# Kernel tuning notes

Hardware: AMD Instinct MI355X
Metric: run time of the kernel (lower is better)

Reference implementation:

```python
import jax, jax.numpy as jnp
import numpy as np

H = 1024      # hidden_size
NH = 16       # num_attention_heads
HD = H // NH  # head_size
DF = 4096     # ff intermediate
EPS = 1e-5


def layer_norm(x, g, b):
    mu = jnp.mean(x, axis=-1, keepdims=True)
    var = jnp.var(x, axis=-1, keepdims=True)
    return (x - mu) * jax.lax.rsqrt(var + EPS) * g + b


def setup_inputs() -> dict:
    key = jax.random.key(0)
    ks = jax.random.split(key, 4)
    s = 0.02
    return {
        "x": jax.random.normal(ks[0], (2, 2048, H), dtype=jnp.float32),
        "w_qkv": jax.random.normal(ks[1], (H, 3 * H), dtype=jnp.float32) * s,
        "ln1_g": jnp.ones((H,), jnp.float32),
        "ln1_b": jnp.zeros((H,), jnp.float32),
        "w1": jax.random.normal(ks[2], (H, DF), dtype=jnp.float32) * s,
        "b1": jnp.zeros((DF,), jnp.float32),
        "w2": jax.random.normal(ks[3], (DF, H), dtype=jnp.float32) * s,
        "b2": jnp.zeros((H,), jnp.float32),
        "ln2_g": jnp.ones((H,), jnp.float32),
        "ln2_b": jnp.zeros((H,), jnp.float32),
    }


def reference(x, w_qkv, ln1_g, ln1_b, w1, b1, w2, b2, ln2_g, ln2_b):
    b, s, h = x.shape
    # --- MHSelfAttention (naive) ---
    qkv = x @ w_qkv                                   # [b, s, 3h]
    qkv = qkv.reshape(b, s, 3, NH, HD)
    q, k, v = (jnp.moveaxis(qkv, 2, 0)                # [3, b, s, nh, hd]
               .transpose(0, 1, 3, 2, 4))             # [3, b, nh, s, hd]
    # NOTE: faithful quirk — scaled by sqrt(hidden_size), not head_size
    scores = jnp.einsum('bnqd,bnkd->bnqk', q, k) / jnp.sqrt(jnp.float32(h))
    probs = jax.nn.softmax(scores, axis=-1)
    ctx = jnp.einsum('bnqk,bnkd->bnqd', probs, v)     # [b, nh, s, hd]
    attn_out = ctx.transpose(0, 2, 1, 3).reshape(b, s, h)
    # post-norm residual (dropout = identity in eval)
    x = x + layer_norm(attn_out, ln1_g, ln1_b)
    # --- FFN ---
    ff = jax.nn.relu(x @ w1 + b1) @ w2 + b2
    x = x + layer_norm(ff, ln2_g, ln2_b)
    return x
```

## Files before the change

kernel.cpp:

```cpp
#include <hip/hip_runtime.h>


typedef unsigned short u16;
typedef unsigned int u32;
typedef __bf16 bf16x8 __attribute__((ext_vector_type(8)));
typedef float f32x4 __attribute__((ext_vector_type(4)));
typedef float f32x16 __attribute__((ext_vector_type(16)));
typedef u32 u32x4 __attribute__((ext_vector_type(4)));
typedef u16 u16x4 __attribute__((ext_vector_type(4)));

__device__ __forceinline__ u16 f2b(float f) {
  u32 u = __builtin_bit_cast(u32, f);
  u += 0x7fffu + ((u >> 16) & 1u);
  return (u16)(u >> 16);
}
__device__ __forceinline__ float b2f(u16 u) {
  return __builtin_bit_cast(float, (u32)u << 16);
}

__device__ __forceinline__ u32 cvtpk(float lo, float hi) {
  u32 r;
  asm("v_cvt_pk_bf16_f32 %0, %1, %2" : "=v"(r) : "v"(lo), "v"(hi));
  return r;
}

__device__ __forceinline__ void gld_lds16(const u16* g, u16* l) {
  __builtin_amdgcn_global_load_lds(
      (const __attribute__((address_space(1))) u32*)g,
      (__attribute__((address_space(3))) u32*)l, 16, 0, 0);
}

__global__ __launch_bounds__(256) void convert_bf16_kernel(
    const float* __restrict__ in, u16* __restrict__ out) {
  const int idx = blockIdx.x * 256 + threadIdx.x;
  float4 v = ((const float4*)in)[idx];
  u16x4 o = { f2b(v.x), f2b(v.y), f2b(v.z), f2b(v.w) };
  ((u16x4*)out)[idx] = o;
}

__global__ __launch_bounds__(256) void transpose_bf16_kernel(
    const float* __restrict__ in, u16* __restrict__ out, int R, int C) {
  __shared__ float tile[32][33];
  const int cb = blockIdx.x * 32, rb = blockIdx.y * 32;
  const int c = threadIdx.x & 31;
  const int r0 = threadIdx.x >> 5;
#pragma unroll
  for (int rr = 0; rr < 32; rr += 8)
    tile[r0 + rr][c] = in[(size_t)(rb + r0 + rr) * C + cb + c];
  __syncthreads();
#pragma unroll
  for (int rr = 0; rr < 32; rr += 8)
    out[(size_t)(cb + r0 + rr) * R + rb + c] = f2b(tile[c][r0 + rr]);
}

__global__ __launch_bounds__(256) void transpose_v_kernel(
    const u16* __restrict__ qkv, u16* __restrict__ vt) {
  __shared__ u16 t[64][70];
  const int bh = blockIdx.x, st = blockIdx.y;
  const int b = bh >> 4, nh = bh & 15;
  const int s0 = st * 64;
  const int r = threadIdx.x >> 3, c = (threadIdx.x & 7) << 3;
  const u16* src = qkv + (size_t)(b * 2048 + s0) * 3072 + 2048 + nh * 64;
#pragma unroll
  for (int rr = 0; rr < 64; rr += 32)
    *(u32x4*)&t[r + rr][c] = *(const u32x4*)(src + (size_t)(r + rr) * 3072 + c);
  __syncthreads();
  u16* dst = vt + ((size_t)bh * 64) * 2048 + s0;
#pragma unroll
  for (int rr = 0; rr < 64; rr += 32) {
    const int d = r + rr;
    u16 tmp[8];
#pragma unroll
    for (int j = 0; j < 8; ++j) tmp[j] = t[c + j][d];
    *(u32x4*)(dst + (size_t)d * 2048 + c) = *(u32x4*)tmp;
  }
}

#define GT(BUF, SBUF, T2, VM)                                                 \
  {                                                                           \
    const u16(*Ab)[32] = As[BUF];                                             \
    const u16(*Bb)[32] = Bs[BUF];                                             \
    bf16x8 af[4], bfr[4];                                                     \
    _Pragma("unroll") for (int nr = 0; nr < 4; ++nr)                          \
        bfr[nr] = *(const bf16x8*)&Bb[wn * 64 + nr * 16 + l16][cRd];          \
    _Pragma("unroll") for (int mr = 0; mr < 4; ++mr)                          \
        af[mr] = *(const bf16x8*)&Ab[wm * 128 + mr * 16 + l16][cRd];          \
    if ((T2) >= 0) {                                                          \
      gld_lds16(Ag + (size_t)(T2) * 32,         &As[SBUF][w * 16][0]);        \
      gld_lds16(Ag + rstep + (size_t)(T2) * 32, &As[SBUF][128 + w * 16][0]);  \
    }                                                                         \
    asm volatile("s_waitcnt lgkmcnt(0)" ::: "memory");                        \
    __builtin_amdgcn_sched_barrier(0);                                        \
    __builtin_amdgcn_s_setprio(1);                                            \
    _Pragma("unroll") for (int mr = 0; mr < 4; ++mr)                          \
        _Pragma("unroll") for (int nr = 0; nr < 4; ++nr)                      \
            acc[mr][nr] = __builtin_amdgcn_mfma_f32_16x16x32_bf16(            \
                af[mr], bfr[nr], acc[mr][nr], 0, 0, 0);                       \
    __builtin_amdgcn_s_setprio(0);                                            \
    _Pragma("unroll") for (int mr = 0; mr < 4; ++mr)                          \
        af[mr] = *(const bf16x8*)&Ab[wm * 128 + 64 + mr * 16 + l16][cRd];     \
    if ((T2) >= 0) {                                                          \
      gld_lds16(Bg + (size_t)(T2) * 32,         &Bs[SBUF][w * 16][0]);        \
      gld_lds16(Bg + rstep + (size_t)(T2) * 32, &Bs[SBUF][128 + w * 16][0]);  \
    }                                                                         \
    asm volatile("s_waitcnt lgkmcnt(0)" ::: "memory");                        \
    __builtin_amdgcn_sched_barrier(0);                                        \
    __builtin_amdgcn_s_setprio(1);                                            \
    _Pragma("unroll") for (int mr = 0; mr < 4; ++mr)                          \
        _Pragma("unroll") for (int nr = 0; nr < 4; ++nr)                      \
            acc[4 + mr][nr] = __builtin_amdgcn_mfma_f32_16x16x32_bf16(        \
                af[mr], bfr[nr], acc[4 + mr][nr], 0, 0, 0);                   \
    __builtin_amdgcn_s_setprio(0);                                            \
    if ((VM) == 4) asm volatile("s_waitcnt vmcnt(4)" ::: "memory");           \
    else if ((VM) == 0) asm volatile("s_waitcnt vmcnt(0)" ::: "memory");      \
    if ((VM) >= 0) __builtin_amdgcn_s_barrier();                              \
  }

__global__ __launch_bounds__(512) void gemm256_kernel(
    const u16* __restrict__ A, const u16* __restrict__ Bt,
    const float* __restrict__ bias, u16* __restrict__ Cb,
    int M, int N, int K, int relu,
    u16* __restrict__ Cb1, u16* __restrict__ Cb2, u16* __restrict__ Cb3) {
  const int nN = N >> 8;
  const int lin = (blockIdx.x & 7) * ((int)gridDim.x >> 3) + (blockIdx.x >> 3);
  const int m0 = (lin / nN) << 8;
  const int n0 = (lin % nN) << 8;
  const int z = blockIdx.y;
  if (z == 1) Cb = Cb1; else if (z == 2) Cb = Cb2; else if (z == 3) Cb = Cb3;

  const int tid = threadIdx.x;
  const int w = tid >> 6, lane = tid & 63;
  const int quad = lane >> 4, l16 = lane & 15;
  const int wm = w >> 2, wn = w & 3;

  __shared__ u16 As[3][256][32];
  __shared__ u16 Bs[3][256][32];

  f32x4 acc[8][4];
#pragma unroll
  for (int i = 0; i < 8; ++i)
#pragma unroll
    for (int j = 0; j < 4; ++j) acc[i][j] = {0.f, 0.f, 0.f, 0.f};

  const int srow = lane >> 2;
  const int scol = (((lane & 3) ^ (srow & 3)) << 3);
  const u16* Ag = A + (size_t)(m0 + w * 16 + srow) * K + (size_t)z * 1024 + scol;
  const u16* Bg = Bt + (size_t)(n0 + w * 16 + srow) * K + (size_t)z * 1024 + scol;
  const size_t rstep = (size_t)128 * K;

  const int cRd = ((quad ^ (l16 & 3)) << 3);

  gld_lds16(Ag,              &As[0][w * 16][0]);
  gld_lds16(Ag + rstep,      &As[0][128 + w * 16][0]);
  gld_lds16(Bg,              &Bs[0][w * 16][0]);
  gld_lds16(Bg + rstep,      &Bs[0][128 + w * 16][0]);
  gld_lds16(Ag + 32,         &As[1][w * 16][0]);
  gld_lds16(Ag + rstep + 32, &As[1][128 + w * 16][0]);
  gld_lds16(Bg + 32,         &Bs[1][w * 16][0]);
  gld_lds16(Bg + rstep + 32, &Bs[1][128 + w * 16][0]);
  asm volatile("s_waitcnt vmcnt(4)" ::: "memory");
  __builtin_amdgcn_s_barrier();

  for (int tt = 0; tt < 10; ++tt) {
    const int t = tt * 3;
    GT(0, 2, t + 2, 4)
    GT(1, 0, t + 3, 4)
    GT(2, 1, t + 4, 4)
  }
  GT(0, 0, -1, 0)
  GT(1, 0, -1, -1)

#pragma unroll
  for (int mr = 0; mr < 8; ++mr) {
    const int row = m0 + wm * 128 + mr * 16 + quad * 4;
#pragma unroll
    for (int nr = 0; nr < 4; ++nr) {
      const int col = n0 + wn * 64 + nr * 16 + l16;
      const float bv = bias ? bias[col] : 0.f;
#pragma unroll
      for (int r = 0; r < 4; ++r) {
        float v = acc[mr][nr][r] + bv;
        if (relu) v = fmaxf(v, 0.f);
        Cb[(size_t)(row + r) * N + col] = f2b(v);
      }
    }
  }
}

__global__ __launch_bounds__(256, 4) void attn_kernel(
    const u16* __restrict__ qkv, const u16* __restrict__ vt,
    float* __restrict__ Op0, float* __restrict__ Op1,
    float* __restrict__ lpart) {
  const int bh = blockIdx.x;
  const int qt = blockIdx.y;
  const int kz = blockIdx.z;
  const int b = bh >> 4, nh = bh & 15;
  const int tid = threadIdx.x;
  const int w = tid >> 6, lane = tid & 63;
  const int l32 = lane & 31, hi = lane >> 5;
  const float c2 = 0.04508422f;

  __shared__ u16 KS[64][64];
  __shared__ u16 VS[64][64];

  const size_t rs = 3072;
  const u16* qbase = qkv + (size_t)b * 2048 * rs + nh * 64;
  const u16* kbase = qbase + 1024;
  const u16* vbase = vt + (size_t)bh * 64 * 2048;
  const int q0 = qt * 128;
  const int k0beg = kz * 1024;

  bf16x8 aq[4];
  {
    const u16* qrow = qbase + (size_t)(q0 + w * 32 + l32) * rs + hi * 8;
#pragma unroll
    for (int ds = 0; ds < 4; ++ds) {
      u32x4 v = *(const u32x4*)(qrow + ds * 16);
      u16 ti[8], to[8];
      *(u32x4*)ti = v;
#pragma unroll
      for (int j = 0; j < 8; ++j) to[j] = f2b(b2f(ti[j]) * c2);
      u32x4 pk = *(u32x4*)to;
      aq[ds] = __builtin_bit_cast(bf16x8, pk);
    }
  }

  f32x16 Oacc[2];
#pragma unroll
  for (int dn = 0; dn < 2; ++dn)
#pragma unroll
    for (int i = 0; i < 16; ++i) Oacc[dn][i] = 0.f;
  float ls[4] = {0.f, 0.f, 0.f, 0.f};

  const int srow = lane >> 3;
  const int scol = ((lane & 7) ^ srow) << 3;

#pragma unroll 1
  for (int t = 0; t < 16; ++t) {
    const int k0 = k0beg + t * 64;
    __syncthreads();
    gld_lds16(kbase + (size_t)(k0 + w * 16 + srow) * rs + scol,       &KS[w * 16][0]);
    gld_lds16(kbase + (size_t)(k0 + w * 16 + 8 + srow) * rs + scol,   &KS[w * 16 + 8][0]);
    gld_lds16(vbase + (size_t)(w * 16 + srow) * 2048 + k0 + scol,     &VS[w * 16][0]);
    gld_lds16(vbase + (size_t)(w * 16 + 8 + srow) * 2048 + k0 + scol, &VS[w * 16 + 8][0]);
    __syncthreads();

    f32x16 S[2];
#pragma unroll
    for (int jt = 0; jt < 2; ++jt)
#pragma unroll
      for (int i = 0; i < 16; ++i) S[jt][i] = 0.f;
#pragma unroll
    for (int jt = 0; jt < 2; ++jt) {
      const int krow = jt * 32 + l32;
#pragma unroll
      for (int ds = 0; ds < 4; ++ds) {
        bf16x8 kv = *(const bf16x8*)&KS[krow][((2 * ds + hi) ^ (krow & 7)) << 3];
        S[jt] = __builtin_amdgcn_mfma_f32_32x32x16_bf16(kv, aq[ds], S[jt], 0, 0, 0);
      }
    }

    bf16x8 pa[4];
#pragma unroll
    for (int jt = 0; jt < 2; ++jt) {
      float p[16];
#pragma unroll
      for (int r = 0; r < 16; ++r) {
        p[r] = exp2f(S[jt][r]);
        ls[r & 3] += p[r];
      }
#pragma unroll
      for (int bq = 0; bq < 2; ++bq) {
        u32 x0 = cvtpk(p[8 * bq + 0], p[8 * bq + 1]);
        u32 y0 = cvtpk(p[8 * bq + 4], p[8 * bq + 5]);
        u32 x1 = cvtpk(p[8 * bq + 2], p[8 * bq + 3]);
        u32 y1 = cvtpk(p[8 * bq + 6], p[8 * bq + 7]);
        asm("v_permlane32_swap_b32 %0, %1" : "+v"(x0), "+v"(y0));
        asm("v_permlane32_swap_b32 %0, %1" : "+v"(x1), "+v"(y1));
        u32x4 dw = {x0, x1, y0, y1};
        pa[2 * jt + bq] = __builtin_bit_cast(bf16x8, dw);
      }
    }

#pragma unroll
    for (int dn = 0; dn < 2; ++dn) {
      const int vrow = dn * 32 + l32;
#pragma unroll
      for (int ks = 0; ks < 4; ++ks) {
        bf16x8 vv = *(const bf16x8*)&VS[vrow][((2 * ks + hi) ^ (vrow & 7)) << 3];
        Oacc[dn] = __builtin_amdgcn_mfma_f32_32x32x16_bf16(pa[ks], vv, Oacc[dn], 0, 0, 0);
      }
    }
  }

  float lsum = (ls[0] + ls[1]) + (ls[2] + ls[3]);
  const float ltot = lsum + __shfl_xor(lsum, 32);

  float* opart = kz ? Op1 : Op0;
  float* obase = opart + (size_t)b * 2048 * 1024 + (size_t)nh * 64;
  float* lbase = lpart + (size_t)kz * 4096 * 16 + (size_t)b * 2048 * 16 + nh;
#pragma unroll
  for (int r = 0; r < 16; ++r) {
    const int qrow = q0 + w * 32 + (r & 3) + 8 * (r >> 2) + 4 * hi;
#pragma unroll
    for (int dn = 0; dn < 2; ++dn)
      obase[(size_t)qrow * 1024 + dn * 32 + l32] = Oacc[dn][r];
  }
  if (lane < 32) lbase[(size_t)(q0 + w * 32 + l32) * 16] = ltot;
}

__global__ __launch_bounds__(256) void ln_attn_kernel(
    const float* __restrict__ O0, const float* __restrict__ O1,
    const float* __restrict__ l0, const float* __restrict__ l1,
    const float* __restrict__ xres, const float* __restrict__ g,
    const float* __restrict__ bb, float* __restrict__ outf,
    u16* __restrict__ outb) {
  const int row = blockIdx.x;
  const int tid = threadIdx.x;
  const int w = tid >> 6, lane = tid & 63;
  const int head = tid >> 4;
  float4 a0 = ((const float4*)(O0 + (size_t)row * 1024))[tid];
  float4 a1 = ((const float4*)(O1 + (size_t)row * 1024))[tid];
  const float inv = 1.f / (l0[row * 16 + head] + l1[row * 16 + head]);
  float4 v;
  v.x = (a0.x + a1.x) * inv;
  v.y = (a0.y + a1.y) * inv;
  v.z = (a0.z + a1.z) * inv;
  v.w = (a0.w + a1.w) * inv;
  float s = v.x + v.y + v.z + v.w;
  float s2 = v.x * v.x + v.y * v.y + v.z * v.z + v.w * v.w;
#pragma unroll
  for (int off = 32; off > 0; off >>= 1) {
    s += __shfl_xor(s, off);
    s2 += __shfl_xor(s2, off);
  }
  __shared__ float red[8];
  if (lane == 0) { red[w] = s; red[4 + w] = s2; }
  __syncthreads();
  s = red[0] + red[1] + red[2] + red[3];
  s2 = red[4] + red[5] + red[6] + red[7];
  const float mu = s * (1.f / 1024.f);
  const float var = s2 * (1.f / 1024.f) - mu * mu;
  const float rstd = rsqrtf(var + 1e-5f);
  float4 xr = ((const float4*)(xres + (size_t)row * 1024))[tid];
  float4 gv = ((const float4*)g)[tid];
  float4 bv = ((const float4*)bb)[tid];
  float4 o;
  o.x = xr.x + (v.x - mu) * rstd * gv.x + bv.x;
  o.y = xr.y + (v.y - mu) * rstd * gv.y + bv.y;
  o.z = xr.z + (v.z - mu) * rstd * gv.z + bv.z;
  o.w = xr.w + (v.w - mu) * rstd * gv.w + bv.w;
  ((float4*)(outf + (size_t)row * 1024))[tid] = o;
  u16x4 ob = { f2b(o.x), f2b(o.y), f2b(o.z), f2b(o.w) };
  *(u16x4*)(outb + (size_t)row * 1024 + (size_t)tid * 4) = ob;
}

__global__ __launch_bounds__(256) void ln_ffn_kernel(
    const u16* __restrict__ p0, const u16* __restrict__ p1,
    const u16* __restrict__ p2, const u16* __restrict__ p3,
    const float* __restrict__ bias, const float* __restrict__ xres,
    const float* __restrict__ g, const float* __restrict__ bb,
    float* __restrict__ outf) {
  const int row = blockIdx.x;
  const int tid = threadIdx.x;
  const int w = tid >> 6, lane = tid & 63;
  u16x4 a0 = ((const u16x4*)(p0 + (size_t)row * 1024))[tid];
  u16x4 a1 = ((const u16x4*)(p1 + (size_t)row * 1024))[tid];
  u16x4 a2 = ((const u16x4*)(p2 + (size_t)row * 1024))[tid];
  u16x4 a3 = ((const u16x4*)(p3 + (size_t)row * 1024))[tid];
  float4 bv4 = ((const float4*)bias)[tid];
  float4 v;
  v.x = (b2f(a0[0]) + b2f(a1[0])) + (b2f(a2[0]) + b2f(a3[0])) + bv4.x;
  v.y = (b2f(a0[1]) + b2f(a1[1])) + (b2f(a2[1]) + b2f(a3[1])) + bv4.y;
  v.z = (b2f(a0[2]) + b2f(a1[2])) + (b2f(a2[2]) + b2f(a3[2])) + bv4.z;
  v.w = (b2f(a0[3]) + b2f(a1[3])) + (b2f(a2[3]) + b2f(a3[3])) + bv4.w;
  float s = v.x + v.y + v.z + v.w;
  float s2 = v.x * v.x + v.y * v.y + v.z * v.z + v.w * v.w;
#pragma unroll
  for (int off = 32; off > 0; off >>= 1) {
    s += __shfl_xor(s, off);
    s2 += __shfl_xor(s2, off);
  }
  __shared__ float red[8];
  if (lane == 0) { red[w] = s; red[4 + w] = s2; }
  __syncthreads();
  s = red[0] + red[1] + red[2] + red[3];
  s2 = red[4] + red[5] + red[6] + red[7];
  const float mu = s * (1.f / 1024.f);
  const float var = s2 * (1.f / 1024.f) - mu * mu;
  const float rstd = rsqrtf(var + 1e-5f);
  float4 xr = ((const float4*)(xres + (size_t)row * 1024))[tid];
  float4 gv = ((const float4*)g)[tid];
  float4 bv = ((const float4*)bb)[tid];
  float4 o;
  o.x = xr.x + (v.x - mu) * rstd * gv.x + bv.x;
  o.y = xr.y + (v.y - mu) * rstd * gv.y + bv.y;
  o.z = xr.z + (v.z - mu) * rstd * gv.z + bv.z;
  o.w = xr.w + (v.w - mu) * rstd * gv.w + bv.w;
  ((float4*)(outf + (size_t)row * 1024))[tid] = o;
}

extern "C" void kernel_launch(void* const* d_in, const int* in_sizes, int n_in,
                              void* d_out, int out_size, void* d_ws, size_t ws_size,
                              hipStream_t stream) {
  const float* x     = (const float*)d_in[0];
  const float* w_qkv = (const float*)d_in[1];
  const float* ln1_g = (const float*)d_in[2];
  const float* ln1_b = (const float*)d_in[3];
  const float* w1    = (const float*)d_in[4];
  const float* b1    = (const float*)d_in[5];
  const float* w2    = (const float*)d_in[6];
  const float* b2    = (const float*)d_in[7];
  const float* ln2_g = (const float*)d_in[8];
  const float* ln2_b = (const float*)d_in[9];
  float* out = (float*)d_out;
  char* ws = (char*)d_ws;

  u16*   xb    = (u16*)(ws + 0);
  u16*   wqkvT = (u16*)(ws + 8388608);
  u16*   qkvb  = (u16*)(ws + 31457280);
  u16*   vT    = (u16*)(ws + 56623104);
  float* Op0   = (float*)(ws + 0);
  float* Op1   = (float*)(ws + 73400320);
  float* lp    = (float*)(ws + 90177536);
  float* x1    = (float*)(ws + 31457280);
  u16*   x1b   = (u16*)(ws + 48234496);
  u16*   w1T   = (u16*)(ws + 14680064);
  u16*   w2T   = (u16*)(ws + 23068672);
  u16*   h1    = (u16*)(ws + 56623104);
  u16*   fp0   = (u16*)(ws + 0);
  u16*   fp1   = (u16*)(ws + 8388608);
  u16*   fp2   = (u16*)(ws + 48234496);
  u16*   fp3   = (u16*)(ws + 90177536);

  convert_bf16_kernel<<<4096, 256, 0, stream>>>(x, xb);
  transpose_bf16_kernel<<<dim3(96, 32), 256, 0, stream>>>(w_qkv, wqkvT, 1024, 3072);

  gemm256_kernel<<<dim3(192, 1), 512, 0, stream>>>(
      xb, wqkvT, nullptr, qkvb, 4096, 3072, 1024, 0,
      nullptr, nullptr, nullptr);
  transpose_v_kernel<<<dim3(32, 32), 256, 0, stream>>>(qkvb, vT);
  attn_kernel<<<dim3(32, 16, 2), 256, 0, stream>>>(qkvb, vT, Op0, Op1, lp);

  ln_attn_kernel<<<4096, 256, 0, stream>>>(
      Op0, Op1, lp, lp + 4096 * 16, x, ln1_g, ln1_b, x1, x1b);

  transpose_bf16_kernel<<<dim3(128, 32), 256, 0, stream>>>(w1, w1T, 1024, 4096);
  transpose_bf16_kernel<<<dim3(32, 128), 256, 0, stream>>>(w2, w2T, 4096, 1024);

  gemm256_kernel<<<dim3(256, 1), 512, 0, stream>>>(
      x1b, w1T, b1, h1, 4096, 4096, 1024, 1,
      nullptr, nullptr, nullptr);
  gemm256_kernel<<<dim3(64, 4), 512, 0, stream>>>(
      h1, w2T, nullptr, fp0, 4096, 1024, 4096, 0,
      fp1, fp2, fp3);

  ln_ffn_kernel<<<4096, 256, 0, stream>>>(
      fp0, fp1, fp2, fp3, b2, x1, ln2_g, ln2_b, out);
}
```

Before: 320.7 us.

## Software-pipeline attention loop with triple-buffered K/V LDS and interleaved QK/softmax/PV

Restructures the attention inner loop into a software pipeline. K/V tiles are prefetched into a triple-buffered LDS ring one tile ahead. Each iteration overlaps softmax of the previous scores, the QK MFMA of the current tile and the PV MFMA of the prior tile, with one barrier instead of two. This raises LDS use and register pressure, and the launch-bounds occupancy hint of 4 is dropped, so occupancy may fall.

```diff
diff --git a/kernel.cpp b/kernel.cpp
--- a/kernel.cpp
+++ b/kernel.cpp
@@ -187,7 +187,55 @@
   }
 }
 
-__global__ __launch_bounds__(256, 4) void attn_kernel(
+
+#define SMAX(SI)                                                              \
+  _Pragma("unroll") for (int jt = 0; jt < 2; ++jt) {                          \
+    float p[16];                                                              \
+    _Pragma("unroll") for (int r = 0; r < 16; ++r) {                          \
+      p[r] = exp2f(SI[jt][r]);                                                \
+      ls[r & 3] += p[r];                                                      \
+    }                                                                         \
+    _Pragma("unroll") for (int bq = 0; bq < 2; ++bq) {                        \
+      u32 x0 = cvtpk(p[8 * bq + 0], p[8 * bq + 1]);                           \
+      u32 y0 = cvtpk(p[8 * bq + 4], p[8 * bq + 5]);                           \
+      u32 x1 = cvtpk(p[8 * bq + 2], p[8 * bq + 3]);                           \
+      u32 y1 = cvtpk(p[8 * bq + 6], p[8 * bq + 7]);                           \
+      asm("v_permlane32_swap_b32 %0, %1" : "+v"(x0), "+v"(y0));               \
+      asm("v_permlane32_swap_b32 %0, %1" : "+v"(x1), "+v"(y1));               \
+      u32x4 dw = {x0, x1, y0, y1};                                            \
+      pa[2 * jt + bq] = __builtin_bit_cast(bf16x8, dw);                       \
+    }                                                                         \
+  }
+
+#define QKM(SO, CUR)                                                          \
+  _Pragma("unroll") for (int jt = 0; jt < 2; ++jt) {                          \
+    _Pragma("unroll") for (int i = 0; i < 16; ++i) SO[jt][i] = 0.f;           \
+    const int krow = jt * 32 + l32;                                           \
+    _Pragma("unroll") for (int ds = 0; ds < 4; ++ds) {                        \
+      bf16x8 kv = *(const bf16x8*)&KS[CUR][krow][((2 * ds + hi) ^ (krow & 7)) << 3]; \
+      SO[jt] = __builtin_amdgcn_mfma_f32_32x32x16_bf16(kv, aq[ds], SO[jt], 0, 0, 0); \
+    }                                                                         \
+  }
+
+#define PVM(PRV)                                                              \
+  _Pragma("unroll") for (int dn = 0; dn < 2; ++dn) {                          \
+    const int vrow = dn * 32 + l32;                                           \
+    _Pragma("unroll") for (int ks = 0; ks < 4; ++ks) {                        \
+      bf16x8 vv = *(const bf16x8*)&VS[PRV][vrow][((2 * ks + hi) ^ (vrow & 7)) << 3]; \
+      Oacc[dn] = __builtin_amdgcn_mfma_f32_32x32x16_bf16(pa[ks], vv, Oacc[dn], 0, 0, 0); \
+    }                                                                         \
+  }
+
+#define AI(SI, SO, CUR, PRV, NXT, KO, LAST)                                   \
+  {                                                                           \
+    if (!(LAST)) stage(NXT, (KO));                                            \
+    SMAX(SI)                                                                  \
+    QKM(SO, CUR)                                                              \
+    PVM(PRV)                                                                  \
+    __syncthreads();                                                          \
+  }
+
+__global__ __launch_bounds__(256) void attn_kernel(
     const u16* __restrict__ qkv, const u16* __restrict__ vt,
     float* __restrict__ Op0, float* __restrict__ Op1,
     float* __restrict__ lpart) {
@@ -200,8 +248,8 @@
   const int l32 = lane & 31, hi = lane >> 5;
   const float c2 = 0.04508422f;
 
-  __shared__ u16 KS[64][64];
-  __shared__ u16 VS[64][64];
+  __shared__ u16 KS[3][64][64];
+  __shared__ u16 VS[3][64][64];
 
   const size_t rs = 3072;
   const u16* qbase = qkv + (size_t)b * 2048 * rs + nh * 64;
@@ -210,6 +258,18 @@
   const int q0 = qt * 128;
   const int k0beg = kz * 1024;
 
+  const int srow = lane >> 3;
+  const int scol = ((lane & 7) ^ srow) << 3;
+
+  auto stage = [&](int buf, int k0) {
+    gld_lds16(kbase + (size_t)(k0 + w * 16 + srow) * rs + scol,       &KS[buf][w * 16][0]);
+    gld_lds16(kbase + (size_t)(k0 + w * 16 + 8 + srow) * rs + scol,   &KS[buf][w * 16 + 8][0]);
+    gld_lds16(vbase + (size_t)(w * 16 + srow) * 2048 + k0 + scol,     &VS[buf][w * 16][0]);
+    gld_lds16(vbase + (size_t)(w * 16 + 8 + srow) * 2048 + k0 + scol, &VS[buf][w * 16 + 8][0]);
+  };
+
+  stage(0, k0beg);
+
   bf16x8 aq[4];
   {
     const u16* qrow = qbase + (size_t)(q0 + w * 32 + l32) * rs + hi * 8;
@@ -231,67 +291,31 @@
 #pragma unroll
     for (int i = 0; i < 16; ++i) Oacc[dn][i] = 0.f;
   float ls[4] = {0.f, 0.f, 0.f, 0.f};
-
-  const int srow = lane >> 3;
-  const int scol = ((lane & 7) ^ srow) << 3;
+  f32x16 SA[2], SB[2];
+  bf16x8 pa[4];
+
+  __syncthreads();
+
+  stage(1, k0beg + 64);
+  QKM(SA, 0)
+  __syncthreads();
 
 #pragma unroll 1
-  for (int t = 0; t < 16; ++t) {
-    const int k0 = k0beg + t * 64;
-    __syncthreads();
-    gld_lds16(kbase + (size_t)(k0 + w * 16 + srow) * rs + scol,       &KS[w * 16][0]);
-    gld_lds16(kbase + (size_t)(k0 + w * 16 + 8 + srow) * rs + scol,   &KS[w * 16 + 8][0]);
-    gld_lds16(vbase + (size_t)(w * 16 + srow) * 2048 + k0 + scol,     &VS[w * 16][0]);
-    gld_lds16(vbase + (size_t)(w * 16 + 8 + srow) * 2048 + k0 + scol, &VS[w * 16 + 8][0]);
-    __syncthreads();
-
-    f32x16 S[2];
-#pragma unroll
-    for (int jt = 0; jt < 2; ++jt)
-#pragma unroll
-      for (int i = 0; i < 16; ++i) S[jt][i] = 0.f;
-#pragma unroll
-    for (int jt = 0; jt < 2; ++jt) {
-      const int krow = jt * 32 + l32;
-#pragma unroll
-      for (int ds = 0; ds < 4; ++ds) {
-        bf16x8 kv = *(const bf16x8*)&KS[krow][((2 * ds + hi) ^ (krow & 7)) << 3];
-        S[jt] = __builtin_amdgcn_mfma_f32_32x32x16_bf16(kv, aq[ds], S[jt], 0, 0, 0);
-      }
-    }
-
-    bf16x8 pa[4];
-#pragma unroll
-    for (int jt = 0; jt < 2; ++jt) {
-      float p[16];
-#pragma unroll
-      for (int r = 0; r < 16; ++r) {
-        p[r] = exp2f(S[jt][r]);
-        ls[r & 3] += p[r];
-      }
-#pragma unroll
-      for (int bq = 0; bq < 2; ++bq) {
-        u32 x0 = cvtpk(p[8 * bq + 0], p[8 * bq + 1]);
-        u32 y0 = cvtpk(p[8 * bq + 4], p[8 * bq + 5]);
-        u32 x1 = cvtpk(p[8 * bq + 2], p[8 * bq + 3]);
-        u32 y1 = cvtpk(p[8 * bq + 6], p[8 * bq + 7]);
-        asm("v_permlane32_swap_b32 %0, %1" : "+v"(x0), "+v"(y0));
-        asm("v_permlane32_swap_b32 %0, %1" : "+v"(x1), "+v"(y1));
-        u32x4 dw = {x0, x1, y0, y1};
-        pa[2 * jt + bq] = __builtin_bit_cast(bf16x8, dw);
-      }
-    }
-
-#pragma unroll
-    for (int dn = 0; dn < 2; ++dn) {
-      const int vrow = dn * 32 + l32;
-#pragma unroll
-      for (int ks = 0; ks < 4; ++ks) {
-        bf16x8 vv = *(const bf16x8*)&VS[vrow][((2 * ks + hi) ^ (vrow & 7)) << 3];
-        Oacc[dn] = __builtin_amdgcn_mfma_f32_32x32x16_bf16(pa[ks], vv, Oacc[dn], 0, 0, 0);
-      }
-    }
-  }
+  for (int g = 0; g < 2; ++g) {
+    const int kg = k0beg + g * 6 * 64;
+    AI(SA, SB, 1, 0, 2, kg + 2 * 64, 0)
+    AI(SB, SA, 2, 1, 0, kg + 3 * 64, 0)
+    AI(SA, SB, 0, 2, 1, kg + 4 * 64, 0)
+    AI(SB, SA, 1, 0, 2, kg + 5 * 64, 0)
+    AI(SA, SB, 2, 1, 0, kg + 6 * 64, 0)
+    AI(SB, SA, 0, 2, 1, kg + 7 * 64, 0)
+  }
+  AI(SA, SB, 1, 0, 2, k0beg + 14 * 64, 0)
+  AI(SB, SA, 2, 1, 0, k0beg + 15 * 64, 0)
+  AI(SA, SB, 0, 2, 1, 0, 1)
+
+  SMAX(SB)
+  PVM(0)
 
   float lsum = (ls[0] + ls[1]) + (ls[2] + ls[3]);
   const float ltot = lsum + __shfl_xor(lsum, 32);
```

Result: no change. 324.2 us (+1.1%).
